# Performance work log

Measured on AMD Instinct MI355X. Metric: run time of the kernel, lower is better.

The kernel has to match this reference:

```python
import jax, jax.numpy as jnp
import numpy as np
import math

NUM_HEADS = 4


def setup_inputs() -> dict:
    key = jax.random.key(0)
    k1, k2, k3, k4 = jax.random.split(key, 4)
    b, c, f, t = 8, 512, 32, 64
    x = jax.random.normal(k1, (b, c, f, t), dtype=jnp.float32)
    # Conv1d(k=1) weights stored as 2D (out, in); fan-in scaled like torch default
    qkv_w = jax.random.normal(k2, (3 * c, c), dtype=jnp.float32) / math.sqrt(c)
    qkv_b = jax.random.normal(k3, (3 * c,), dtype=jnp.float32) * 0.02
    proj_w = jax.random.normal(k4, (c, c), dtype=jnp.float32) / math.sqrt(c)
    proj_b = jnp.zeros((c,), dtype=jnp.float32)
    return {"x": x, "qkv_w": qkv_w, "qkv_b": qkv_b, "proj_w": proj_w, "proj_b": proj_b}


def reference(x, qkv_w, qkv_b, proj_w, proj_b):
    b, c, f, t = x.shape
    T = f * t
    xr = x.reshape(b, c, T)  # [b, c, T]
    # Note: original forward computes PositionalEncoding2D(x) but discards it.
    qkv = jnp.einsum('oc,bct->bot', qkv_w, xr) + qkv_b[None, :, None]  # [b, 3c, T]
    H = NUM_HEADS
    ch = c // H
    q, k, v = jnp.split(qkv, 3, axis=1)  # each [b, c, T]
    q = q.reshape(b * H, ch, T)
    k = k.reshape(b * H, ch, T)
    v = v.reshape(b * H, ch, T)
    scale = 1.0 / math.sqrt(math.sqrt(ch))
    w = jnp.einsum('bct,bcs->bts', q * scale, k * scale)  # [b*H, T, T]
    w = jax.nn.softmax(w.astype(jnp.float32), axis=-1).astype(q.dtype)
    a = jnp.einsum('bts,bcs->bct', w, v).reshape(b, c, T)
    h = jnp.einsum('oc,bct->bot', proj_w, a) + proj_b[None, :, None]
    return (xr + h).reshape(b, c, f, t)
```

## Files before the change

kernel.cpp:

```cpp
#include <hip/hip_runtime.h>

#define DEV static __device__ __forceinline__

typedef __attribute__((ext_vector_type(8))) short short8;
typedef __attribute__((ext_vector_type(4))) float f32x4;
typedef __attribute__((ext_vector_type(16))) float f32x16;

DEV unsigned short f2bf(float f) {
    union { float f; unsigned int u; } v; v.f = f;
    unsigned int u = v.u;
    unsigned int r = (u + 0x7fffu + ((u >> 16) & 1u)) >> 16;
    return (unsigned short)r;
}

DEV unsigned int cvtpk(float lo, float hi) {
    unsigned int r;
    asm("v_cvt_pk_bf16_f32 %0, %1, %2" : "=v"(r) : "v"(lo), "v"(hi));
    return r;
}

DEV unsigned short* swp(unsigned short* base, int row, int col, int rs) {
    int a = ((row * rs + col) << 1) ^ ((row & 7) << 4);
    return (unsigned short*)((char*)base + a);
}

__global__ void prep_kernel(const float* __restrict__ qkv_w,
                            const float* __restrict__ proj_w,
                            unsigned short* __restrict__ Wq,
                            unsigned short* __restrict__ Wp) {
    int i = blockIdx.x * blockDim.x + threadIdx.x;
    int stride = gridDim.x * blockDim.x;
    for (int j = i; j < 1536 * 512; j += stride) Wq[j] = f2bf(qkv_w[j]);
    for (int j = i; j < 512 * 512;  j += stride) Wp[j] = f2bf(proj_w[j]);
}

__global__ __launch_bounds__(256) void transpose_kernel(const float* __restrict__ x,
                                                        unsigned short* __restrict__ Xt) {
    __shared__ unsigned char lt[64 * 128];
    int b  = blockIdx.z;
    int c0 = blockIdx.y * 64;
    int t0 = blockIdx.x * 64;
    int tid = threadIdx.x;
    int tx = tid & 15, cy0 = tid >> 4;
    for (int p = 0; p < 4; ++p) {
        int cy = cy0 + p * 16;
        const float* src = &x[((size_t)(b * 512 + c0 + cy)) * 2048 + t0 + tx * 4];
        f32x4 v = *(const f32x4*)src;
        unsigned long long pk = (unsigned long long)f2bf(v[0])
                              | ((unsigned long long)f2bf(v[1]) << 16)
                              | ((unsigned long long)f2bf(v[2]) << 32)
                              | ((unsigned long long)f2bf(v[3]) << 48);
        int addr = (cy * 128 + tx * 8) ^ ((cy & 7) << 4);
        *(unsigned long long*)(lt + addr) = pk;
    }
    __syncthreads();
    int c16 = (tid & 3) * 16, tr = tid >> 2;
    unsigned short buf[16];
    for (int i = 0; i < 16; ++i) {
        int c = c16 + i;
        int addr = (c * 128 + tr * 2) ^ ((c & 7) << 4);
        buf[i] = *(unsigned short*)(lt + addr);
    }
    unsigned short* dst = &Xt[((size_t)(b * 2048 + t0 + tr)) * 512 + c0 + c16];
    *(short8*)dst       = *(short8*)&buf[0];
    *(short8*)(dst + 8) = *(short8*)&buf[8];
}

#define LP 72

template <int ORIENT>
__global__ __launch_bounds__(256, 2) void gemm_qkv_kernel(
    const unsigned short* __restrict__ Wq,
    const unsigned short* __restrict__ Xt,
    const float* __restrict__ qkv_b,
    unsigned short* __restrict__ Qw,
    unsigned short* __restrict__ Kw,
    unsigned short* __restrict__ Vw) {
    __shared__ unsigned short Ws[128][LP];
    __shared__ unsigned short Bs[128][LP];
    int b  = blockIdx.z;
    int ot = (ORIENT == 0) ? blockIdx.y : (8 + blockIdx.y);
    int o0 = ot * 128, t0 = blockIdx.x * 128;
    int tid = threadIdx.x, lane = tid & 63, w = tid >> 6;
    int lr = lane >> 4, lc = lane & 15;
    int wr = (w >> 1) * 64, wc = (w & 1) * 64;
    f32x4 acc[4][4];
    for (int m = 0; m < 4; m++)
        for (int n = 0; n < 4; n++) acc[m][n] = (f32x4){0.f, 0.f, 0.f, 0.f};
    int srow = tid >> 3, soff = (tid & 7) * 8;
    for (int k0 = 0; k0 < 512; k0 += 64) {
        __syncthreads();
        for (int rr = srow; rr < 128; rr += 32) {
            *(short8*)&Ws[rr][soff] = *(const short8*)&Wq[(size_t)(o0 + rr) * 512 + k0 + soff];
            *(short8*)&Bs[rr][soff] = *(const short8*)&Xt[((size_t)(b * 2048) + t0 + rr) * 512 + k0 + soff];
        }
        __syncthreads();
        for (int kk = 0; kk < 64; kk += 32) {
            int kb = kk + lr * 8;
            short8 af[4], bfv[4];
            if (ORIENT == 0) {
                for (int m = 0; m < 4; m++) af[m]  = *(const short8*)&Bs[wr + m * 16 + lc][kb];
                for (int n = 0; n < 4; n++) bfv[n] = *(const short8*)&Ws[wc + n * 16 + lc][kb];
            } else {
                for (int m = 0; m < 4; m++) af[m]  = *(const short8*)&Ws[wr + m * 16 + lc][kb];
                for (int n = 0; n < 4; n++) bfv[n] = *(const short8*)&Bs[wc + n * 16 + lc][kb];
            }
            for (int m = 0; m < 4; m++)
                for (int n = 0; n < 4; n++)
                    acc[m][n] = __builtin_amdgcn_mfma_f32_16x16x32_bf16(af[m], bfv[n], acc[m][n], 0, 0, 0);
        }
    }
    const float scale = 0.29730177875068026f;
    for (int m = 0; m < 4; m++)
        for (int n = 0; n < 4; n++)
            for (int r = 0; r < 4; r++) {
                int row = wr + m * 16 + lr * 4 + r;
                int col = wc + n * 16 + lc;
                float val = acc[m][n][r];
                if (ORIENT == 0) {
                    int t = t0 + row;
                    int o = o0 + col;
                    val = (val + qkv_b[o]) * scale;
                    if (o < 512) {
                        int h = o >> 7, cc = o & 127;
                        Qw[((size_t)((b * 4 + h) * 2048 + t)) * 128 + cc] = f2bf(val);
                    } else {
                        int oo = o - 512;
                        int h = oo >> 7, cc = oo & 127;
                        Kw[((size_t)((b * 4 + h) * 2048 + t)) * 128 + cc] = f2bf(val);
                    }
                } else {
                    int o = o0 + row;
                    int t = t0 + col;
                    val += qkv_b[o];
                    int oo = o - 1024;
                    int h = oo >> 7, cc = oo & 127;
                    Vw[((size_t)((b * 4 + h) * 128 + cc)) * 2048 + t] = f2bf(val);
                }
            }
}

__global__ __launch_bounds__(512, 2) void attn_kernel(
    const unsigned short* __restrict__ Qw,
    const unsigned short* __restrict__ Kw,
    const unsigned short* __restrict__ Vw,
    unsigned short* __restrict__ Aw) {
    __shared__ unsigned short lds[32768];
    int bid = blockIdx.x;
    int bh = bid & 31;
    int t0 = (bid >> 5) * 256;
    int tid = threadIdx.x, lane = tid & 63, w = tid >> 6;
    int l31 = lane & 31, hi = lane >> 5;
    int qrow = w * 32;

    const unsigned short* Kbase = &Kw[(size_t)bh * 2048 * 128];
    const unsigned short* Vbase = &Vw[(size_t)bh * 128 * 2048];

    short8 qf[8];
    #pragma unroll
    for (int st = 0; st < 8; st++)
        qf[st] = *(const short8*)&Qw[((size_t)bh * 2048 + t0 + qrow + l31) * 128 + st * 16 + hi * 8];

    f32x16 oacc[4];
    #pragma unroll
    for (int ct = 0; ct < 4; ct++)
        #pragma unroll
        for (int i = 0; i < 16; i++) oacc[ct][i] = 0.f;
    float mst = -1e30f, lst = 0.f;

    int kr = tid >> 4, ko = (tid & 15) * 8;
    int vr = tid >> 3, vo = (tid & 7) * 8;

    short8 kreg[2], vreg[2];
    #pragma unroll
    for (int p = 0; p < 2; p++)
        kreg[p] = *(const short8*)&Kbase[(size_t)(kr + p * 32) * 128 + ko];
    #pragma unroll
    for (int p = 0; p < 2; p++)
        vreg[p] = *(const short8*)&Vbase[(size_t)(vr + p * 64) * 2048 + vo];

    for (int it = 0; it < 32; ++it) {
        int cur = it & 1;
        unsigned short* Kb = lds + cur * 8192;
        unsigned short* Vb = lds + 16384 + cur * 8192;
        #pragma unroll
        for (int p = 0; p < 2; p++) *(short8*)swp(Kb, kr + p * 32, ko, 128) = kreg[p];
        #pragma unroll
        for (int p = 0; p < 2; p++) *(short8*)swp(Vb, vr + p * 64, vo, 64) = vreg[p];
        if (it + 1 < 32) {
            int s1 = (it + 1) * 64;
            #pragma unroll
            for (int p = 0; p < 2; p++)
                kreg[p] = *(const short8*)&Kbase[(size_t)(s1 + kr + p * 32) * 128 + ko];
            #pragma unroll
            for (int p = 0; p < 2; p++)
                vreg[p] = *(const short8*)&Vbase[(size_t)(vr + p * 64) * 2048 + s1 + vo];
        }
        __syncthreads();

        f32x16 s0, s1v;
        #pragma unroll
        for (int i = 0; i < 16; i++) { s0[i] = 0.f; s1v[i] = 0.f; }
        __builtin_amdgcn_s_setprio(1);
        #pragma unroll
        for (int st = 0; st < 8; st++) {
            short8 k0 = *(const short8*)swp(Kb, l31,      st * 16 + hi * 8, 128);
            short8 k1 = *(const short8*)swp(Kb, 32 + l31, st * 16 + hi * 8, 128);
            s0  = __builtin_amdgcn_mfma_f32_32x32x16_bf16(k0, qf[st], s0, 0, 0, 0);
            s1v = __builtin_amdgcn_mfma_f32_32x32x16_bf16(k1, qf[st], s1v, 0, 0, 0);
        }
        __builtin_amdgcn_s_setprio(0);

        float m16[16];
        #pragma unroll
        for (int i = 0; i < 16; i++) m16[i] = fmaxf(s0[i], s1v[i]);
        #pragma unroll
        for (int sdt = 8; sdt > 0; sdt >>= 1)
            #pragma unroll
            for (int i = 0; i < 8; i++)
                if (i < sdt) m16[i] = fmaxf(m16[i], m16[i + sdt]);
        float mx = fmaxf(m16[0], __shfl_xor(m16[0], 32, 64));
        float mnew = fmaxf(mst, mx);
        float resc = __expf(mst - mnew);
        mst = mnew;
        float pe[32];
        #pragma unroll
        for (int i = 0; i < 16; i++) pe[i]      = __expf(s0[i]  - mnew);
        #pragma unroll
        for (int i = 0; i < 16; i++) pe[16 + i] = __expf(s1v[i] - mnew);
        float a16[16];
        #pragma unroll
        for (int i = 0; i < 16; i++) a16[i] = pe[i] + pe[16 + i];
        #pragma unroll
        for (int sdt = 8; sdt > 0; sdt >>= 1)
            #pragma unroll
            for (int i = 0; i < 8; i++)
                if (i < sdt) a16[i] = a16[i] + a16[i + sdt];
        float rs = a16[0] + __shfl_xor(a16[0], 32, 64);
        lst = lst * resc + rs;
        #pragma unroll
        for (int ct = 0; ct < 4; ct++)
            #pragma unroll
            for (int i = 0; i < 16; i++) oacc[ct][i] *= resc;

        short8 pf[4];
        #pragma unroll
        for (int st = 0; st < 4; st++) {
            unsigned X0 = cvtpk(pe[st * 8 + 0], pe[st * 8 + 1]);
            unsigned X1 = cvtpk(pe[st * 8 + 2], pe[st * 8 + 3]);
            unsigned Y0 = cvtpk(pe[st * 8 + 4], pe[st * 8 + 5]);
            unsigned Y1 = cvtpk(pe[st * 8 + 6], pe[st * 8 + 7]);
            unsigned Xp0 = (unsigned)__shfl_xor((int)X0, 32, 64);
            unsigned Xp1 = (unsigned)__shfl_xor((int)X1, 32, 64);
            unsigned Yp0 = (unsigned)__shfl_xor((int)Y0, 32, 64);
            unsigned Yp1 = (unsigned)__shfl_xor((int)Y1, 32, 64);
            union { unsigned u[4]; short8 s; } uu;
            uu.u[0] = hi ? Yp0 : X0;
            uu.u[1] = hi ? Yp1 : X1;
            uu.u[2] = hi ? Y0  : Xp0;
            uu.u[3] = hi ? Y1  : Xp1;
            pf[st] = uu.s;
        }

        __builtin_amdgcn_s_setprio(1);
        #pragma unroll
        for (int ct = 0; ct < 4; ct++)
            #pragma unroll
            for (int st = 0; st < 4; st++) {
                short8 va = *(const short8*)swp(Vb, ct * 32 + l31, st * 16 + hi * 8, 64);
                oacc[ct] = __builtin_amdgcn_mfma_f32_32x32x16_bf16(va, pf[st], oacc[ct], 0, 0, 0);
            }
        __builtin_amdgcn_s_setprio(0);
    }

    __syncthreads();
    unsigned short* ep = lds + w * 4096;
    float invl = 1.f / lst;
    #pragma unroll
    for (int ct = 0; ct < 4; ct++)
        #pragma unroll
        for (int i = 0; i < 8; i++) {
            int c = (2 * i & 3) + 8 * (i >> 1) + 4 * hi + 32 * ct;
            unsigned d = cvtpk(oacc[ct][2 * i] * invl, oacc[ct][2 * i + 1] * invl);
            *(unsigned*)swp(ep, l31, c, 128) = d;
        }
    asm volatile("" ::: "memory");
    int q = lane >> 1, hf = lane & 1;
    int b = bh >> 2, h = bh & 3;
    #pragma unroll
    for (int p = 0; p < 8; p++) {
        short8 v = *(const short8*)swp(ep, q, hf * 64 + p * 8, 128);
        *(short8*)&Aw[((size_t)(b * 2048) + t0 + qrow + q) * 512 + h * 128 + hf * 64 + p * 8] = v;
    }
}

__global__ __launch_bounds__(256, 2) void gemm_proj_kernel(
    const unsigned short* __restrict__ Wp,
    const unsigned short* __restrict__ Aw,
    const float* __restrict__ proj_b,
    const float* __restrict__ x,
    float* __restrict__ out) {
    __shared__ unsigned short Ws[128][LP];
    __shared__ unsigned short Bs[128][LP];
    int b  = blockIdx.z;
    int o0 = blockIdx.y * 128, t0 = blockIdx.x * 128;
    int tid = threadIdx.x, lane = tid & 63, w = tid >> 6;
    int lr = lane >> 4, lc = lane & 15;
    int wr = (w >> 1) * 64, wc = (w & 1) * 64;
    f32x4 acc[4][4];
    for (int m = 0; m < 4; m++)
        for (int n = 0; n < 4; n++) acc[m][n] = (f32x4){0.f, 0.f, 0.f, 0.f};
    int srow = tid >> 3, soff = (tid & 7) * 8;
    for (int k0 = 0; k0 < 512; k0 += 64) {
        __syncthreads();
        for (int rr = srow; rr < 128; rr += 32) {
            *(short8*)&Ws[rr][soff] = *(const short8*)&Wp[(size_t)(o0 + rr) * 512 + k0 + soff];
            *(short8*)&Bs[rr][soff] = *(const short8*)&Aw[((size_t)(b * 2048) + t0 + rr) * 512 + k0 + soff];
        }
        __syncthreads();
        for (int kk = 0; kk < 64; kk += 32) {
            int kb = kk + lr * 8;
            short8 af[4], bfv[4];
            for (int m = 0; m < 4; m++) af[m]  = *(const short8*)&Ws[wr + m * 16 + lc][kb];
            for (int n = 0; n < 4; n++) bfv[n] = *(const short8*)&Bs[wc + n * 16 + lc][kb];
            for (int m = 0; m < 4; m++)
                for (int n = 0; n < 4; n++)
                    acc[m][n] = __builtin_amdgcn_mfma_f32_16x16x32_bf16(af[m], bfv[n], acc[m][n], 0, 0, 0);
        }
    }
    for (int m = 0; m < 4; m++)
        for (int n = 0; n < 4; n++)
            for (int r = 0; r < 4; r++) {
                int o = o0 + wr + m * 16 + lr * 4 + r;
                int t = t0 + wc + n * 16 + lc;
                size_t idx = ((size_t)(b * 512) + o) * 2048 + t;
                out[idx] = x[idx] + acc[m][n][r] + proj_b[o];
            }
}

extern "C" void kernel_launch(void* const* d_in, const int* in_sizes, int n_in,
                              void* d_out, int out_size, void* d_ws, size_t ws_size,
                              hipStream_t stream) {
    const float* x      = (const float*)d_in[0];
    const float* qkv_w  = (const float*)d_in[1];
    const float* qkv_b  = (const float*)d_in[2];
    const float* proj_w = (const float*)d_in[3];
    const float* proj_b = (const float*)d_in[4];
    float* out = (float*)d_out;

    unsigned short* ws = (unsigned short*)d_ws;
    unsigned short* Wq = ws;
    unsigned short* Wp = Wq + (size_t)1536 * 512;
    unsigned short* Xt = Wp + (size_t)512 * 512;
    unsigned short* Qw = Xt + (size_t)8 * 2048 * 512;
    unsigned short* Kw = Qw + (size_t)32 * 2048 * 128;
    unsigned short* Vw = Kw + (size_t)32 * 2048 * 128;
    unsigned short* Aw = Vw + (size_t)32 * 2048 * 128;

    prep_kernel<<<dim3(512), dim3(256), 0, stream>>>(qkv_w, proj_w, Wq, Wp);
    transpose_kernel<<<dim3(32, 8, 8), dim3(256), 0, stream>>>(x, Xt);
    gemm_qkv_kernel<0><<<dim3(16, 8, 8), dim3(256), 0, stream>>>(Wq, Xt, qkv_b, Qw, Kw, Vw);
    gemm_qkv_kernel<1><<<dim3(16, 4, 8), dim3(256), 0, stream>>>(Wq, Xt, qkv_b, Qw, Kw, Vw);
    attn_kernel<<<dim3(256), dim3(512), 0, stream>>>(Qw, Kw, Vw, Aw);
    gemm_proj_kernel<<<dim3(16, 4, 8), dim3(256), 0, stream>>>(Wp, Aw, proj_b, x, out);
}
```

Baseline: 178.6 us.

## Merge QKV GEMM launches, use permlane32 swaps, and defer softmax rescaling

Merges the two templated QKV GEMM launches into one grid that picks its orientation at runtime from blockIdx.y, removing a launch and the gap between them. In the attention kernel, the cross-half-wave shuffles for the row max, row sum and P-fragment packing are replaced with permlane32_swap. The running-max rescale of the output accumulators is skipped unless the new max exceeds the stored one by more than a threshold of 8, which cuts multiplies and exps per tile. The deferred rescale relies on exp values up to e^8 staying in range for bf16 and fp32. Runtime orientation selection in the GEMM adds pointer selects and branches.

```diff
diff --git a/kernel.cpp b/kernel.cpp
--- a/kernel.cpp
+++ b/kernel.cpp
@@ -5,6 +5,7 @@
 typedef __attribute__((ext_vector_type(8))) short short8;
 typedef __attribute__((ext_vector_type(4))) float f32x4;
 typedef __attribute__((ext_vector_type(16))) float f32x16;
+typedef __attribute__((ext_vector_type(2))) unsigned int uint2v;
 
 DEV unsigned short f2bf(float f) {
     union { float f; unsigned int u; } v; v.f = f;
@@ -17,6 +18,19 @@
     unsigned int r;
     asm("v_cvt_pk_bf16_f32 %0, %1, %2" : "=v"(r) : "v"(lo), "v"(hi));
     return r;
+}
+
+DEV float pl32_max(float v) {
+    union { float f; unsigned u; } c; c.f = v;
+    uint2v r = __builtin_amdgcn_permlane32_swap(c.u, c.u, false, false);
+    union { unsigned u; float f; } a, b; a.u = r[0]; b.u = r[1];
+    return fmaxf(a.f, b.f);
+}
+DEV float pl32_sum(float v) {
+    union { float f; unsigned u; } c; c.f = v;
+    uint2v r = __builtin_amdgcn_permlane32_swap(c.u, c.u, false, false);
+    union { unsigned u; float f; } a, b; a.u = r[0]; b.u = r[1];
+    return a.f + b.f;
 }
 
 DEV unsigned short* swp(unsigned short* base, int row, int col, int rs) {
@@ -68,7 +82,6 @@
 
 #define LP 72
 
-template <int ORIENT>
 __global__ __launch_bounds__(256, 2) void gemm_qkv_kernel(
     const unsigned short* __restrict__ Wq,
     const unsigned short* __restrict__ Xt,
@@ -79,7 +92,8 @@
     __shared__ unsigned short Ws[128][LP];
     __shared__ unsigned short Bs[128][LP];
     int b  = blockIdx.z;
-    int ot = (ORIENT == 0) ? blockIdx.y : (8 + blockIdx.y);
+    int ot = blockIdx.y;
+    bool orient0 = (ot < 8);
     int o0 = ot * 128, t0 = blockIdx.x * 128;
     int tid = threadIdx.x, lane = tid & 63, w = tid >> 6;
     int lr = lane >> 4, lc = lane & 15;
@@ -88,6 +102,9 @@
     for (int m = 0; m < 4; m++)
         for (int n = 0; n < 4; n++) acc[m][n] = (f32x4){0.f, 0.f, 0.f, 0.f};
     int srow = tid >> 3, soff = (tid & 7) * 8;
+    typedef unsigned short (*lds_t)[LP];
+    lds_t Aarr = orient0 ? (lds_t)Bs : (lds_t)Ws;
+    lds_t Barr = orient0 ? (lds_t)Ws : (lds_t)Bs;
     for (int k0 = 0; k0 < 512; k0 += 64) {
         __syncthreads();
         for (int rr = srow; rr < 128; rr += 32) {
@@ -98,13 +115,8 @@
         for (int kk = 0; kk < 64; kk += 32) {
             int kb = kk + lr * 8;
             short8 af[4], bfv[4];
-            if (ORIENT == 0) {
-                for (int m = 0; m < 4; m++) af[m]  = *(const short8*)&Bs[wr + m * 16 + lc][kb];
-                for (int n = 0; n < 4; n++) bfv[n] = *(const short8*)&Ws[wc + n * 16 + lc][kb];
-            } else {
-                for (int m = 0; m < 4; m++) af[m]  = *(const short8*)&Ws[wr + m * 16 + lc][kb];
-                for (int n = 0; n < 4; n++) bfv[n] = *(const short8*)&Bs[wc + n * 16 + lc][kb];
-            }
+            for (int m = 0; m < 4; m++) af[m]  = *(const short8*)&Aarr[wr + m * 16 + lc][kb];
+            for (int n = 0; n < 4; n++) bfv[n] = *(const short8*)&Barr[wc + n * 16 + lc][kb];
             for (int m = 0; m < 4; m++)
                 for (int n = 0; n < 4; n++)
                     acc[m][n] = __builtin_amdgcn_mfma_f32_16x16x32_bf16(af[m], bfv[n], acc[m][n], 0, 0, 0);
@@ -117,7 +129,7 @@
                 int row = wr + m * 16 + lr * 4 + r;
                 int col = wc + n * 16 + lc;
                 float val = acc[m][n][r];
-                if (ORIENT == 0) {
+                if (orient0) {
                     int t = t0 + row;
                     int o = o0 + col;
                     val = (val + qkv_b[o]) * scale;
@@ -219,15 +231,22 @@
             #pragma unroll
             for (int i = 0; i < 8; i++)
                 if (i < sdt) m16[i] = fmaxf(m16[i], m16[i + sdt]);
-        float mx = fmaxf(m16[0], __shfl_xor(m16[0], 32, 64));
-        float mnew = fmaxf(mst, mx);
-        float resc = __expf(mst - mnew);
-        mst = mnew;
+        float mx = pl32_max(m16[0]);
+        if (!__all(mx <= mst + 8.0f)) {
+            float mnew = fmaxf(mst, mx);
+            float resc = __expf(mst - mnew);
+            mst = mnew;
+            lst *= resc;
+            #pragma unroll
+            for (int ct = 0; ct < 4; ct++)
+                #pragma unroll
+                for (int i = 0; i < 16; i++) oacc[ct][i] *= resc;
+        }
         float pe[32];
         #pragma unroll
-        for (int i = 0; i < 16; i++) pe[i]      = __expf(s0[i]  - mnew);
-        #pragma unroll
-        for (int i = 0; i < 16; i++) pe[16 + i] = __expf(s1v[i] - mnew);
+        for (int i = 0; i < 16; i++) pe[i]      = __expf(s0[i]  - mst);
+        #pragma unroll
+        for (int i = 0; i < 16; i++) pe[16 + i] = __expf(s1v[i] - mst);
         float a16[16];
         #pragma unroll
         for (int i = 0; i < 16; i++) a16[i] = pe[i] + pe[16 + i];
@@ -236,12 +255,7 @@
             #pragma unroll
             for (int i = 0; i < 8; i++)
                 if (i < sdt) a16[i] = a16[i] + a16[i + sdt];
-        float rs = a16[0] + __shfl_xor(a16[0], 32, 64);
-        lst = lst * resc + rs;
-        #pragma unroll
-        for (int ct = 0; ct < 4; ct++)
-            #pragma unroll
-            for (int i = 0; i < 16; i++) oacc[ct][i] *= resc;
+        lst += pl32_sum(a16[0]);
 
         short8 pf[4];
         #pragma unroll
@@ -250,15 +264,13 @@
             unsigned X1 = cvtpk(pe[st * 8 + 2], pe[st * 8 + 3]);
             unsigned Y0 = cvtpk(pe[st * 8 + 4], pe[st * 8 + 5]);
             unsigned Y1 = cvtpk(pe[st * 8 + 6], pe[st * 8 + 7]);
-            unsigned Xp0 = (unsigned)__shfl_xor((int)X0, 32, 64);
-            unsigned Xp1 = (unsigned)__shfl_xor((int)X1, 32, 64);
-            unsigned Yp0 = (unsigned)__shfl_xor((int)Y0, 32, 64);
-            unsigned Yp1 = (unsigned)__shfl_xor((int)Y1, 32, 64);
+            uint2v r0 = __builtin_amdgcn_permlane32_swap(X0, Y0, false, false);
+            uint2v r1 = __builtin_amdgcn_permlane32_swap(X1, Y1, false, false);
             union { unsigned u[4]; short8 s; } uu;
-            uu.u[0] = hi ? Yp0 : X0;
-            uu.u[1] = hi ? Yp1 : X1;
-            uu.u[2] = hi ? Y0  : Xp0;
-            uu.u[3] = hi ? Y1  : Xp1;
+            uu.u[0] = r0[0];
+            uu.u[1] = r1[0];
+            uu.u[2] = r0[1];
+            uu.u[3] = r1[1];
             pf[st] = uu.s;
         }
 
@@ -359,8 +371,7 @@
 
     prep_kernel<<<dim3(512), dim3(256), 0, stream>>>(qkv_w, proj_w, Wq, Wp);
     transpose_kernel<<<dim3(32, 8, 8), dim3(256), 0, stream>>>(x, Xt);
-    gemm_qkv_kernel<0><<<dim3(16, 8, 8), dim3(256), 0, stream>>>(Wq, Xt, qkv_b, Qw, Kw, Vw);
-    gemm_qkv_kernel<1><<<dim3(16, 4, 8), dim3(256), 0, stream>>>(Wq, Xt, qkv_b, Qw, Kw, Vw);
+    gemm_qkv_kernel<<<dim3(16, 12, 8), dim3(256), 0, stream>>>(Wq, Xt, qkv_b, Qw, Kw, Vw);
     attn_kernel<<<dim3(256), dim3(512), 0, stream>>>(Qw, Kw, Vw, Aw);
     gemm_proj_kernel<<<dim3(16, 4, 8), dim3(256), 0, stream>>>(Wp, Aw, proj_b, x, out);
 }
```

Measured after the change: 301.7 us. +68.9%, slower.
